# Kernel tuning notes

Hardware: AMD Instinct MI355X
Metric: run time of the kernel (lower is better)

Reference implementation:

```python
import jax, jax.numpy as jnp
import numpy as np

N = 30000   # nodes
E = 600000  # edges (avg degree 20)
H = 128     # hidden_channels
L = 4       # num_layers
G = 64      # graphs in batch


def _init(key, shape, fan_in):
    return (jax.random.normal(key, shape, jnp.float32) / np.sqrt(fan_in)).astype(jnp.float32)


def setup_inputs() -> dict:
    key = jax.random.key(0)
    ks = jax.random.split(key, 24)
    x = jax.random.normal(ks[0], (N, 1), jnp.float32)
    pos = jax.random.normal(ks[1], (N, 3), jnp.float32)
    edge_index = jax.random.randint(ks[2], (2, E), 0, N, dtype=jnp.int32).astype(jnp.int64)
    batch = jnp.sort(jax.random.randint(ks[3], (N,), 0, G, dtype=jnp.int32)).astype(jnp.int64)

    emb_w = _init(ks[4], (1, H), 1)
    emb_b = jnp.zeros((H,), jnp.float32)

    # stacked per-layer params: msg MLP (2H+1 -> H -> H), node MLP (2H -> H -> H)
    msg_w1 = _init(ks[5], (L, 2 * H + 1, H), 2 * H + 1)
    msg_b1 = jnp.zeros((L, H), jnp.float32)
    msg_w2 = _init(ks[6], (L, H, H), H)
    msg_b2 = jnp.zeros((L, H), jnp.float32)
    node_w1 = _init(ks[7], (L, 2 * H, H), 2 * H)
    node_b1 = jnp.zeros((L, H), jnp.float32)
    node_w2 = _init(ks[8], (L, H, H), H)
    node_b2 = jnp.zeros((L, H), jnp.float32)

    out_w1 = _init(ks[9], (H, 32), H)
    out_b1 = jnp.zeros((32,), jnp.float32)
    out_w2 = _init(ks[10], (32, 1), 32)
    out_b2 = jnp.zeros((1,), jnp.float32)

    return {
        "x": x, "pos": pos, "edge_index": edge_index, "batch": batch,
        "emb_w": emb_w, "emb_b": emb_b,
        "msg_w1": msg_w1, "msg_b1": msg_b1, "msg_w2": msg_w2, "msg_b2": msg_b2,
        "node_w1": node_w1, "node_b1": node_b1, "node_w2": node_w2, "node_b2": node_b2,
        "out_w1": out_w1, "out_b1": out_b1, "out_w2": out_w2, "out_b2": out_b2,
    }


def reference(x, pos, edge_index, batch,
              emb_w, emb_b,
              msg_w1, msg_b1, msg_w2, msg_b2,
              node_w1, node_b1, node_w2, node_b2,
              out_w1, out_b1, out_w2, out_b2):
    row, col = edge_index[0], edge_index[1]  # row = source j, col = target i
    # edge scalar: squared distance (computed once, reused across layers)
    dist_sq = jnp.sum((pos[row] - pos[col]) ** 2, axis=-1, keepdims=True)  # [E,1]

    h = x @ emb_w + emb_b  # [N,H]
    for l in range(L):
        x_j = h[row]   # source features
        x_i = h[col]   # target features
        m = jnp.concatenate([x_i, x_j, dist_sq], axis=-1)           # [E, 2H+1]
        m = jax.nn.silu(m @ msg_w1[l] + msg_b1[l]) @ msg_w2[l] + msg_b2[l]  # [E,H]
        aggr = jax.ops.segment_sum(m, col, num_segments=N)          # scatter-add to targets
        nh = jnp.concatenate([h, aggr], axis=-1)                    # [N, 2H]
        h = jax.nn.silu(nh @ node_w1[l] + node_b1[l]) @ node_w2[l] + node_b2[l]
        # dropout omitted for deterministic reference (eval mode)

    g = jax.ops.segment_sum(h, batch, num_segments=G)               # global_add_pool [G,H]
    return jax.nn.silu(g @ out_w1 + out_b1) @ out_w2 + out_b2       # [G,1]
```

## Files before the change

kernel.cpp:

```cpp
#include <hip/hip_runtime.h>

typedef unsigned short u16;
typedef __bf16 bf16x8 __attribute__((ext_vector_type(8)));
typedef float f32x4 __attribute__((ext_vector_type(4)));

#define HN 128
#define TM 64
#define ASTRIDE 136
#define ECH 256

__device__ __forceinline__ u16 f2bf(float f) {
  union { float f; unsigned u; } v; v.f = f;
  unsigned r = v.u + 0x7fffu + ((v.u >> 16) & 1u);
  return (u16)(r >> 16);
}
__device__ __forceinline__ float bf2f(u16 v) {
  union { unsigned u; float f; } x; x.u = ((unsigned)v) << 16; return x.f;
}
__device__ __forceinline__ float bflo(unsigned v) {
  union { unsigned u; float f; } x; x.u = v << 16; return x.f;
}
__device__ __forceinline__ float bfhi(unsigned v) {
  union { unsigned u; float f; } x; x.u = v & 0xffff0000u; return x.f;
}
__device__ __forceinline__ float silu_f(float x) {
  float e = __builtin_amdgcn_exp2f(-1.442695041f * x);
  return x * __builtin_amdgcn_rcpf(1.f + e);
}

__global__ void pack_weights(const float* __restrict__ msg_w1, const float* __restrict__ msg_w2,
                             const float* __restrict__ node_w1, const float* __restrict__ node_w2,
                             u16* __restrict__ pw, int* __restrict__ deg,
                             float* __restrict__ g, int N_, int GH) {
  int id = blockIdx.x * 256 + threadIdx.x;
  if (id < N_) deg[id] = 0;
  if (id < GH) g[id] = 0.f;
  if (id >= 4 * 6 * 16384) return;
  int l = id / (6 * 16384);
  int rem = id % (6 * 16384);
  int m = rem / 16384;
  int e = rem % 16384;
  int kg = e >> 10;
  int n = (e >> 3) & 127;
  int j = e & 7;
  int k = kg * 8 + j;
  float v = 0.f;
  switch (m) {
    case 0: v = msg_w1[(l * 257 + k) * 128 + n]; break;
    case 1: v = msg_w1[(l * 257 + 128 + k) * 128 + n]; break;
    case 2: v = msg_w2[(l * 128 + k) * 128 + n]; break;
    case 3: v = node_w1[(l * 256 + k) * 128 + n]; break;
    case 4: v = node_w1[(l * 256 + 128 + k) * 128 + n]; break;
    case 5: v = node_w2[(l * 128 + k) * 128 + n]; break;
  }
  pw[id] = f2bf(v);
}

__device__ __forceinline__ void gemm64(const u16* s_A, const u16* s_W,
                                       int w, int quad, int m16, f32x4 acc[8]) {
#pragma unroll
  for (int ks = 0; ks < 4; ks++) {
    bf16x8 a = *(const bf16x8*)&s_A[(w * 16 + m16) * ASTRIDE + ks * 32 + quad * 8];
#pragma unroll
    for (int ct = 0; ct < 8; ct++) {
      bf16x8 b = *(const bf16x8*)&s_W[(ks * 4 + quad) * 1024 + (ct * 16 + m16) * 8];
      acc[ct] = __builtin_amdgcn_mfma_f32_16x16x32_bf16(a, b, acc[ct], 0, 0, 0);
    }
  }
}

__global__ __launch_bounds__(256) void fold_kernel(
    const float* __restrict__ msg_w2, const float* __restrict__ node_w1,
    const float* __restrict__ msg_b2, const u16* __restrict__ pw,
    u16* __restrict__ pwc, float* __restrict__ vc) {
  __shared__ __align__(16) u16 s_A[TM * ASTRIDE];
  __shared__ __align__(16) u16 s_W[16384];
  const int t = threadIdx.x;
  const int w = t >> 6, lane = t & 63, quad = lane >> 4, m16 = lane & 15;
  const int b = blockIdx.x, l = b >> 1, half = b & 1;
  const int tile0 = half * 64;

  {
    int r = t >> 2, qo = (t & 3) * 32;
    const float4* src = (const float4*)(msg_w2 + (size_t)(l * 128 + tile0 + r) * 128 + qo);
    u16* dst = s_A + r * ASTRIDE + qo;
#pragma unroll
    for (int i = 0; i < 8; i++) {
      float4 v = src[i];
      ushort4 o;
      o.x = f2bf(v.x); o.y = f2bf(v.y); o.z = f2bf(v.z); o.w = f2bf(v.w);
      *(ushort4*)(dst + i * 4) = o;
    }
  }
  {
    const int4* src = (const int4*)(pw + (size_t)(l * 6 + 4) * 16384);
    int4* dst = (int4*)s_W;
#pragma unroll
    for (int i = 0; i < 8; i++) dst[t + i * 256] = src[t + i * 256];
  }
  __syncthreads();
  f32x4 acc[8];
#pragma unroll
  for (int ct = 0; ct < 8; ct++) acc[ct] = {0.f, 0.f, 0.f, 0.f};
  gemm64(s_A, s_W, w, quad, m16, acc);
#pragma unroll
  for (int ct = 0; ct < 8; ct++)
#pragma unroll
    for (int j = 0; j < 4; j++) {
      int k = tile0 + w * 16 + quad * 4 + j;
      int n = ct * 16 + m16;
      pwc[(size_t)l * 16384 + (k >> 3) * 1024 + n * 8 + (k & 7)] = f2bf(acc[ct][j]);
    }
  if (half == 0 && t < 128) {
    float s = 0.f;
    for (int np = 0; np < 128; np++)
      s += msg_b2[l * 128 + np] * node_w1[(size_t)(l * 256 + 128 + np) * 128 + t];
    vc[l * 128 + t] = s;
  }
}

__global__ void hist_kernel(const int* __restrict__ eidx, int* __restrict__ deg, int E_) {
  int e = blockIdx.x * 256 + threadIdx.x;
  if (e < E_) atomicAdd(&deg[eidx[E_ + e]], 1);
}

__global__ void scan1_kernel(const int* __restrict__ deg, int* __restrict__ off,
                             int* __restrict__ bsum, int n) {
  __shared__ int s[256];
  int t = threadIdx.x;
  int i = blockIdx.x * 256 + t;
  int v = (i < n) ? deg[i] : 0;
  s[t] = v;
  for (int d = 1; d < 256; d <<= 1) {
    __syncthreads();
    int x = (t >= d) ? s[t - d] : 0;
    __syncthreads();
    s[t] += x;
  }
  __syncthreads();
  if (i < n) off[i] = s[t] - v;
  if (t == 255) bsum[blockIdx.x] = s[255];
}

__global__ void scan2_kernel(int* __restrict__ bsum, int nb) {
  __shared__ int s[256];
  int t = threadIdx.x;
  int v = (t < nb) ? bsum[t] : 0;
  s[t] = v;
  for (int d = 1; d < 256; d <<= 1) {
    __syncthreads();
    int x = (t >= d) ? s[t - d] : 0;
    __syncthreads();
    s[t] += x;
  }
  __syncthreads();
  if (t < nb) bsum[t] = s[t] - v;
}

__global__ void scan3_kernel(int* __restrict__ off, const int* __restrict__ bsum,
                             int* __restrict__ cursor, int n) {
  int i = blockIdx.x * 256 + threadIdx.x;
  if (i < n) {
    int v = off[i] + bsum[blockIdx.x];
    off[i] = v;
    cursor[i] = v;
  }
}

__global__ void scatter_kernel(const int* __restrict__ eidx, const float* __restrict__ pos,
                               int* __restrict__ cursor, int4* __restrict__ es16, int E_) {
  int e = blockIdx.x * 256 + threadIdx.x;
  if (e >= E_) return;
  int sr = eidx[e], tg = eidx[E_ + e];
  float dx = pos[sr * 3 + 0] - pos[tg * 3 + 0];
  float dy = pos[sr * 3 + 1] - pos[tg * 3 + 1];
  float dz = pos[sr * 3 + 2] - pos[tg * 3 + 2];
  float d = dx * dx + dy * dy + dz * dz;
  int p = atomicAdd(&cursor[tg], 1);
  int4 v;
  v.x = sr; v.y = tg; v.z = __float_as_int(d); v.w = 0;
  es16[p] = v;
}

__global__ __launch_bounds__(256) void proj_kernel(
    const float* __restrict__ x, const float* __restrict__ emb_w,
    const float* __restrict__ emb_b, u16* __restrict__ hbf,
    u16* __restrict__ Pout, u16* __restrict__ Qout,
    const u16* __restrict__ pw, const float* __restrict__ b1, int nnodes) {
  __shared__ __align__(16) u16 s_A[TM * ASTRIDE];
  __shared__ __align__(16) u16 s_W[16384];
  const int t = threadIdx.x;
  const int w = t >> 6, lane = t & 63, quad = lane >> 4, m16 = lane & 15;
  const int tile0 = blockIdx.x * TM;
  {
    int r = t >> 2, qo = (t & 3) * 32;
    int node = tile0 + r;
    if (node >= nnodes) node = nnodes - 1;
    float xv = x[node];
    u16 hv[32];
#pragma unroll
    for (int i = 0; i < 32; i++) hv[i] = f2bf(xv * emb_w[qo + i] + emb_b[qo + i]);
    u16* dst = s_A + r * ASTRIDE + qo;
#pragma unroll
    for (int i = 0; i < 4; i++) *(int4*)(dst + i * 8) = *(int4*)(hv + i * 8);
    u16* gd = hbf + (size_t)node * HN + qo;
#pragma unroll
    for (int i = 0; i < 4; i++) *(int4*)(gd + i * 8) = *(int4*)(hv + i * 8);
  }
  {
    const int4* src = (const int4*)pw;
    int4* dst = (int4*)s_W;
#pragma unroll
    for (int i = 0; i < 8; i++) dst[t + i * 256] = src[t + i * 256];
  }
  __syncthreads();
  f32x4 acc[8];
#pragma unroll
  for (int ct = 0; ct < 8; ct++) acc[ct] = {0.f, 0.f, 0.f, 0.f};
  gemm64(s_A, s_W, w, quad, m16, acc);
  __syncthreads();
  {
    const int4* src = (const int4*)(pw + 16384);
    int4* dst = (int4*)s_W;
#pragma unroll
    for (int i = 0; i < 8; i++) dst[t + i * 256] = src[t + i * 256];
  }
  float bb[8];
#pragma unroll
  for (int ct = 0; ct < 8; ct++) bb[ct] = b1[ct * 16 + m16];
#pragma unroll
  for (int ct = 0; ct < 8; ct++)
#pragma unroll
    for (int j = 0; j < 4; j++) {
      int n = tile0 + w * 16 + quad * 4 + j;
      if (n < nnodes) Pout[n * HN + ct * 16 + m16] = f2bf(acc[ct][j] + bb[ct]);
    }
  __syncthreads();
#pragma unroll
  for (int ct = 0; ct < 8; ct++) acc[ct] = {0.f, 0.f, 0.f, 0.f};
  gemm64(s_A, s_W, w, quad, m16, acc);
#pragma unroll
  for (int ct = 0; ct < 8; ct++)
#pragma unroll
    for (int j = 0; j < 4; j++) {
      int n = tile0 + w * 16 + quad * 4 + j;
      if (n < nnodes) Qout[n * HN + ct * 16 + m16] = f2bf(acc[ct][j]);
    }
}

__device__ __forceinline__ void edge_step(
    int tg_s, float dd_s, unsigned qv,
    int& cur_s, float& p0, float& p1, float& s0, float& s1,
    const u16* __restrict__ P, float* __restrict__ S, int cp,
    float wd0, float wd1, int tprev_s, int tnext_s) {
  if (tg_s != cur_s) {
    if (cur_s >= 0) {
      float* dst = &S[(size_t)cur_s * HN + cp];
      if (cur_s == tprev_s || cur_s == tnext_s) {
        atomicAdd(dst, s0);
        atomicAdd(dst + 1, s1);
      } else {
        float2 v = {s0, s1};
        *(float2*)dst = v;
      }
    }
    cur_s = tg_s; s0 = 0.f; s1 = 0.f;
    int cg = tg_s < 0 ? 0 : tg_s;
    unsigned pv = *(const unsigned*)&P[(size_t)cg * HN + cp];
    p0 = bflo(pv); p1 = bfhi(pv);
  }
  float x0 = p0 + bflo(qv) + dd_s * wd0;
  float x1 = p1 + bfhi(qv) + dd_s * wd1;
  s0 += silu_f(x0);
  s1 += silu_f(x1);
}

__global__ __launch_bounds__(256) void edge_kernel(
    const u16* __restrict__ P, const u16* __restrict__ Q,
    float* __restrict__ S, const float* __restrict__ w1d,
    const int4* __restrict__ es16, int E_) {
  __shared__ int s_src[ECH + 8];
  __shared__ int s_tgt[ECH + 8];
  __shared__ float s_dist[ECH + 8];

  const int t = threadIdx.x;
  const int e0 = blockIdx.x * ECH;
  {
    int e = e0 + t;
    if (e < E_) {
      int4 v = es16[e];
      s_src[t] = v.x;
      s_tgt[t] = v.y;
      s_dist[t] = __int_as_float(v.z);
    } else {
      s_src[t] = 0; s_tgt[t] = -1; s_dist[t] = 0.f;
    }
    if (t < 8) { s_src[ECH + t] = 0; s_tgt[ECH + t] = -1; s_dist[ECH + t] = 0.f; }
  }
  __syncthreads();

  const int lane = t & 63;
  const int w = t >> 6;
  const int cp = lane * 2;
  const int a = w * 64;
  const float2 wdv = *(const float2*)&w1d[cp];
  const float wd0 = wdv.x, wd1 = wdv.y;

  int tprev_s, tnext_s;
  if (w == 0) tprev_s = (e0 > 0) ? es16[e0 - 1].y : -2;
  else tprev_s = s_tgt[a - 1];
  if (w == 3) tnext_s = (e0 + ECH < E_) ? es16[e0 + ECH].y : -2;
  else tnext_s = s_tgt[a + 64];
  tprev_s = __builtin_amdgcn_readfirstlane(tprev_s);
  tnext_s = __builtin_amdgcn_readfirstlane(tnext_s);

  int tg[8];
  float dd[8];
  unsigned qv[8];
#pragma unroll
  for (int j = 0; j < 8; j++) {
    tg[j] = s_tgt[a + j];
    dd[j] = s_dist[a + j];
    qv[j] = *(const unsigned*)&Q[(size_t)s_src[a + j] * HN + cp];
  }

  int cur_s = -1;
  float s0 = 0.f, s1 = 0.f, p0 = 0.f, p1 = 0.f;

#pragma unroll
  for (int i = a; i < a + 64; i += 8) {
    int tgn[8];
    float ddn[8];
    unsigned qvn[8];
#pragma unroll
    for (int j = 0; j < 8; j++) {
      int idx = i + 8 + j;
      tgn[j] = s_tgt[idx];
      ddn[j] = s_dist[idx];
      qvn[j] = *(const unsigned*)&Q[(size_t)s_src[idx] * HN + cp];
    }
#pragma unroll
    for (int j = 0; j < 8; j++) {
      int tg_s = __builtin_amdgcn_readfirstlane(tg[j]);
      float dd_s = __builtin_amdgcn_readfirstlane(__float_as_int(dd[j])) != 0
                       ? dd[j] : dd[j];
      edge_step(tg_s, dd[j], qv[j], cur_s, p0, p1, s0, s1, P, S, cp, wd0, wd1, tprev_s, tnext_s);
      (void)dd_s;
    }
#pragma unroll
    for (int j = 0; j < 8; j++) { tg[j] = tgn[j]; dd[j] = ddn[j]; qv[j] = qvn[j]; }
  }

  if (cur_s >= 0) {
    float* dst = &S[(size_t)cur_s * HN + cp];
    if (cur_s == tprev_s || cur_s == tnext_s) {
      atomicAdd(dst, s0);
      atomicAdd(dst + 1, s1);
    } else {
      float2 v = {s0, s1};
      *(float2*)dst = v;
    }
  }
}

template <bool FUSE>
__global__ __launch_bounds__(256) void node_kernel(
    const u16* __restrict__ hbf, float* __restrict__ S, const int* __restrict__ deg,
    u16* __restrict__ hout, const u16* __restrict__ pwc, const float* __restrict__ vc,
    const u16* __restrict__ pwn, const float* __restrict__ b1, const float* __restrict__ b2,
    const u16* __restrict__ pw_next, const float* __restrict__ b1_next,
    u16* __restrict__ Pout, u16* __restrict__ Qout, int nnodes) {
  __shared__ __align__(16) u16 s_A[TM * ASTRIDE];
  __shared__ __align__(16) u16 s_W[16384];
  const int t = threadIdx.x;
  const int w = t >> 6, lane = t & 63, quad = lane >> 4, m16 = lane & 15;
  const int tile0 = blockIdx.x * TM;
  const int r_ = t >> 2, qo_ = (t & 3) * 32;
  int node_ = tile0 + r_;
  if (node_ >= nnodes) node_ = nnodes - 1;

  {
    const int4* src = (const int4*)pwc;
    int4* dst = (int4*)s_W;
#pragma unroll
    for (int i = 0; i < 8; i++) dst[t + i * 256] = src[t + i * 256];
  }
  {
    const float4* src = (const float4*)(S + (size_t)node_ * HN + qo_);
    u16* dst = s_A + r_ * ASTRIDE + qo_;
#pragma unroll
    for (int i = 0; i < 8; i++) {
      float4 v = src[i];
      ushort4 o;
      o.x = f2bf(v.x); o.y = f2bf(v.y); o.z = f2bf(v.z); o.w = f2bf(v.w);
      *(ushort4*)(dst + i * 4) = o;
    }
    float4 z = {0.f, 0.f, 0.f, 0.f};
    float4* zd = (float4*)(S + (size_t)node_ * HN + qo_);
#pragma unroll
    for (int i = 0; i < 8; i++) zd[i] = z;
  }
  __syncthreads();

  f32x4 acc[8];
#pragma unroll
  for (int ct = 0; ct < 8; ct++) acc[ct] = {0.f, 0.f, 0.f, 0.f};
  gemm64(s_A, s_W, w, quad, m16, acc);
  __syncthreads();

  {
    const int4* src = (const int4*)pwn;
    int4* dst = (int4*)s_W;
#pragma unroll
    for (int i = 0; i < 8; i++) dst[t + i * 256] = src[t + i * 256];
  }
  {
    const int4* src = (const int4*)(hbf + (size_t)node_ * HN + qo_);
    int4* dst = (int4*)(s_A + r_ * ASTRIDE + qo_);
#pragma unroll
    for (int i = 0; i < 4; i++) dst[i] = src[i];
  }
  __syncthreads();
  gemm64(s_A, s_W, w, quad, m16, acc);
  __syncthreads();

  {
    const int4* src = (const int4*)(pwn + 32768);
    int4* dst = (int4*)s_W;
#pragma unroll
    for (int i = 0; i < 8; i++) dst[t + i * 256] = src[t + i * 256];
  }
  {
    float bb1[8], vcr[8];
#pragma unroll
    for (int ct = 0; ct < 8; ct++) {
      bb1[ct] = b1[ct * 16 + m16];
      vcr[ct] = vc[ct * 16 + m16];
    }
    float degv[4];
#pragma unroll
    for (int j = 0; j < 4; j++) {
      int n = tile0 + w * 16 + quad * 4 + j;
      if (n >= nnodes) n = nnodes - 1;
      degv[j] = (float)deg[n];
    }
#pragma unroll
    for (int ct = 0; ct < 8; ct++)
#pragma unroll
      for (int j = 0; j < 4; j++) {
        int row = w * 16 + quad * 4 + j;
        float xv = acc[ct][j] + bb1[ct] + degv[j] * vcr[ct];
        s_A[row * ASTRIDE + ct * 16 + m16] = f2bf(silu_f(xv));
      }
  }
  __syncthreads();

#pragma unroll
  for (int ct = 0; ct < 8; ct++) acc[ct] = {0.f, 0.f, 0.f, 0.f};
  gemm64(s_A, s_W, w, quad, m16, acc);

  float bb2[8];
#pragma unroll
  for (int ct = 0; ct < 8; ct++) bb2[ct] = b2[ct * 16 + m16];
#pragma unroll
  for (int ct = 0; ct < 8; ct++)
#pragma unroll
    for (int j = 0; j < 4; j++) {
      int row = w * 16 + quad * 4 + j;
      int n = tile0 + row;
      if (n < nnodes) hout[n * HN + ct * 16 + m16] = f2bf(acc[ct][j] + bb2[ct]);
    }

  if (FUSE) {
#pragma unroll
    for (int ct = 0; ct < 8; ct++)
#pragma unroll
      for (int j = 0; j < 4; j++) {
        int row = w * 16 + quad * 4 + j;
        s_A[row * ASTRIDE + ct * 16 + m16] = f2bf(acc[ct][j] + bb2[ct]);
      }
    __syncthreads();
    {
      const int4* src = (const int4*)pw_next;
      int4* dst = (int4*)s_W;
#pragma unroll
      for (int i = 0; i < 8; i++) dst[t + i * 256] = src[t + i * 256];
    }
    __syncthreads();
#pragma unroll
    for (int ct = 0; ct < 8; ct++) acc[ct] = {0.f, 0.f, 0.f, 0.f};
    gemm64(s_A, s_W, w, quad, m16, acc);
    {
      float bbn[8];
#pragma unroll
      for (int ct = 0; ct < 8; ct++) bbn[ct] = b1_next[ct * 16 + m16];
#pragma unroll
      for (int ct = 0; ct < 8; ct++)
#pragma unroll
        for (int j = 0; j < 4; j++) {
          int n = tile0 + w * 16 + quad * 4 + j;
          if (n < nnodes) Pout[n * HN + ct * 16 + m16] = f2bf(acc[ct][j] + bbn[ct]);
        }
    }
    __syncthreads();
    {
      const int4* src = (const int4*)(pw_next + 16384);
      int4* dst = (int4*)s_W;
#pragma unroll
      for (int i = 0; i < 8; i++) dst[t + i * 256] = src[t + i * 256];
    }
    __syncthreads();
#pragma unroll
    for (int ct = 0; ct < 8; ct++) acc[ct] = {0.f, 0.f, 0.f, 0.f};
    gemm64(s_A, s_W, w, quad, m16, acc);
#pragma unroll
    for (int ct = 0; ct < 8; ct++)
#pragma unroll
      for (int j = 0; j < 4; j++) {
        int n = tile0 + w * 16 + quad * 4 + j;
        if (n < nnodes) Qout[n * HN + ct * 16 + m16] = f2bf(acc[ct][j]);
      }
  }
}

__global__ __launch_bounds__(256) void pool_kernel(
    const u16* __restrict__ h, const int* __restrict__ batch,
    float* __restrict__ g, int N) {
  __shared__ int s_b[64];
  const int t = threadIdx.x;
  const int n0 = blockIdx.x * 64;
  if (t < 64) {
    int n = n0 + t;
    s_b[t] = (n < N) ? batch[n] : -1;
  }
  __syncthreads();
  const int cp = (t & 63) * 2;
  const int rg = t >> 6;
  int cur = -1;
  float s0 = 0.f, s1 = 0.f;
#pragma unroll 4
  for (int i = 0; i < 16; i++) {
    int r = rg * 16 + i;
    int b = s_b[r];
    if (b < 0) break;
    if (b != cur) {
      if (cur >= 0) {
        atomicAdd(&g[cur * HN + cp], s0);
        atomicAdd(&g[cur * HN + cp + 1], s1);
      }
      cur = b; s0 = 0.f; s1 = 0.f;
    }
    unsigned v = *(const unsigned*)&h[(size_t)(n0 + r) * HN + cp];
    s0 += bf2f((u16)(v & 0xffffu));
    s1 += bf2f((u16)(v >> 16));
  }
  if (cur >= 0) {
    atomicAdd(&g[cur * HN + cp], s0);
    atomicAdd(&g[cur * HN + cp + 1], s1);
  }
}

__global__ __launch_bounds__(64) void out_kernel(
    const float* __restrict__ g, const float* __restrict__ w1,
    const float* __restrict__ b1, const float* __restrict__ w2,
    const float* __restrict__ b2, float* __restrict__ out) {
  const int gi = blockIdx.x;
  const int t = threadIdx.x;
  const int c = t & 31, kh = t >> 5;
  float s = 0.f;
  for (int k = kh * 64; k < kh * 64 + 64; k++)
    s += g[gi * HN + k] * w1[k * 32 + c];
  s += __shfl_down(s, 32);
  float r = 0.f;
  if (kh == 0) r = silu_f(s + b1[c]) * w2[c];
  r += __shfl_down(r, 16);
  r += __shfl_down(r, 8);
  r += __shfl_down(r, 4);
  r += __shfl_down(r, 2);
  r += __shfl_down(r, 1);
  if (t == 0) out[gi] = r + b2[0];
}

extern "C" void kernel_launch(void* const* d_in, const int* in_sizes, int n_in,
                              void* d_out, int out_size, void* d_ws, size_t ws_size,
                              hipStream_t stream) {
  const float* x = (const float*)d_in[0];
  const float* pos = (const float*)d_in[1];
  const int* eidx = (const int*)d_in[2];
  const int* batch = (const int*)d_in[3];
  const float* emb_w = (const float*)d_in[4];
  const float* emb_b = (const float*)d_in[5];
  const float* msg_w1 = (const float*)d_in[6];
  const float* msg_b1 = (const float*)d_in[7];
  const float* msg_w2 = (const float*)d_in[8];
  const float* msg_b2 = (const float*)d_in[9];
  const float* node_w1 = (const float*)d_in[10];
  const float* node_b1 = (const float*)d_in[11];
  const float* node_w2 = (const float*)d_in[12];
  const float* node_b2 = (const float*)d_in[13];
  const float* out_w1 = (const float*)d_in[14];
  const float* out_b1 = (const float*)d_in[15];
  const float* out_w2 = (const float*)d_in[16];
  const float* out_b2 = (const float*)d_in[17];
  float* outp = (float*)d_out;

  const int N = 30000, E = 600000, G = 64;
  const size_t NH = (size_t)N * HN;

  u16* hA = (u16*)d_ws;
  u16* hB = hA + NH;
  u16* Pp = hB + NH;
  u16* Qp = Pp + NH;
  float* S = (float*)(Qp + NH);
  int4* es16 = (int4*)(S + NH);
  int* deg = (int*)(es16 + E);
  int* off = deg + N;
  int* cursor = off + N;
  int* bsum = cursor + N;
  float* g = (float*)(bsum + 128);
  u16* pw = (u16*)(g + G * HN);
  u16* pwc = pw + (size_t)4 * 6 * 16384;
  float* vcb = (float*)(pwc + (size_t)4 * 16384);

  const int NB = (N + 255) / 256;
  const int NTB = (N + TM - 1) / TM;

  pack_weights<<<(4 * 6 * 16384 + 255) / 256, 256, 0, stream>>>(
      msg_w1, msg_w2, node_w1, node_w2, pw, deg, g, N, G * HN);
  fold_kernel<<<8, 256, 0, stream>>>(msg_w2, node_w1, msg_b2, pw, pwc, vcb);

  hist_kernel<<<(E + 255) / 256, 256, 0, stream>>>(eidx, deg, E);
  scan1_kernel<<<NB, 256, 0, stream>>>(deg, off, bsum, N);
  scan2_kernel<<<1, 256, 0, stream>>>(bsum, NB);
  scan3_kernel<<<NB, 256, 0, stream>>>(off, bsum, cursor, N);
  scatter_kernel<<<(E + 255) / 256, 256, 0, stream>>>(eidx, pos, cursor, es16, E);

  hipMemsetAsync(S, 0, NH * sizeof(float), stream);

  proj_kernel<<<NTB, 256, 0, stream>>>(x, emb_w, emb_b, hA, Pp, Qp, pw, msg_b1, N);

  u16* hcur = hA;
  u16* hnext = hB;
  for (int l = 0; l < 4; l++) {
    const u16* pwl = pw + (size_t)(l * 6) * 16384;
    edge_kernel<<<(E + ECH - 1) / ECH, 256, 0, stream>>>(
        Pp, Qp, S,
        msg_w1 + (size_t)(l * 257 + 256) * 128,
        es16, E);
    if (l < 3) {
      const u16* pw_next = pw + (size_t)((l + 1) * 6) * 16384;
      node_kernel<true><<<NTB, 256, 0, stream>>>(
          hcur, S, deg, hnext, pwc + (size_t)l * 16384, vcb + l * 128,
          pwl + 3 * 16384, node_b1 + l * 128, node_b2 + l * 128,
          pw_next, msg_b1 + (l + 1) * 128, Pp, Qp, N);
    } else {
      node_kernel<false><<<NTB, 256, 0, stream>>>(
          hcur, S, deg, hnext, pwc + (size_t)l * 16384, vcb + l * 128,
          pwl + 3 * 16384, node_b1 + l * 128, node_b2 + l * 128,
          nullptr, nullptr, nullptr, nullptr, N);
    }
    u16* tmp = hcur; hcur = hnext; hnext = tmp;
  }

  pool_kernel<<<(N + 63) / 64, 256, 0, stream>>>(hcur, batch, g, N);
  out_kernel<<<G, 64, 0, stream>>>(g, out_w1, out_b1, out_w2, out_b2, outp);
}
```

Baseline: 420.0 us.

## Fuse edge aggregation into node kernel with shared-memory CSR accumulation

Merges the separate edge kernel into the per-layer node kernel. Each 64-node tile walks its CSR edge range and accumulates messages into a shared-memory buffer with LDS atomics, replacing the global S buffer, its memset and the global atomics. P/Q are double-buffered because the fused kernel now writes next-layer projections while other blocks still read the current ones. Per-block edge work is now tied to the tile's degree sum, and each wave handles only a quarter of the tile's edges, which may lower latency hiding compared with the old edge-parallel grid.

```diff
diff --git a/kernel.cpp b/kernel.cpp
--- a/kernel.cpp
+++ b/kernel.cpp
@@ -7,7 +7,7 @@
 #define HN 128
 #define TM 64
 #define ASTRIDE 136
-#define ECH 256
+#define SSTRIDE 132
 
 __device__ __forceinline__ u16 f2bf(float f) {
   union { float f; unsigned u; } v; v.f = f;
@@ -248,157 +248,113 @@
     }
 }
 
-__device__ __forceinline__ void edge_step(
-    int tg_s, float dd_s, unsigned qv,
-    int& cur_s, float& p0, float& p1, float& s0, float& s1,
-    const u16* __restrict__ P, float* __restrict__ S, int cp,
-    float wd0, float wd1, int tprev_s, int tnext_s) {
-  if (tg_s != cur_s) {
-    if (cur_s >= 0) {
-      float* dst = &S[(size_t)cur_s * HN + cp];
-      if (cur_s == tprev_s || cur_s == tnext_s) {
-        atomicAdd(dst, s0);
-        atomicAdd(dst + 1, s1);
-      } else {
-        float2 v = {s0, s1};
-        *(float2*)dst = v;
-      }
-    }
-    cur_s = tg_s; s0 = 0.f; s1 = 0.f;
-    int cg = tg_s < 0 ? 0 : tg_s;
-    unsigned pv = *(const unsigned*)&P[(size_t)cg * HN + cp];
-    p0 = bflo(pv); p1 = bfhi(pv);
-  }
-  float x0 = p0 + bflo(qv) + dd_s * wd0;
-  float x1 = p1 + bfhi(qv) + dd_s * wd1;
-  s0 += silu_f(x0);
-  s1 += silu_f(x1);
-}
-
-__global__ __launch_bounds__(256) void edge_kernel(
-    const u16* __restrict__ P, const u16* __restrict__ Q,
-    float* __restrict__ S, const float* __restrict__ w1d,
-    const int4* __restrict__ es16, int E_) {
-  __shared__ int s_src[ECH + 8];
-  __shared__ int s_tgt[ECH + 8];
-  __shared__ float s_dist[ECH + 8];
-
-  const int t = threadIdx.x;
-  const int e0 = blockIdx.x * ECH;
-  {
-    int e = e0 + t;
-    if (e < E_) {
-      int4 v = es16[e];
-      s_src[t] = v.x;
-      s_tgt[t] = v.y;
-      s_dist[t] = __int_as_float(v.z);
-    } else {
-      s_src[t] = 0; s_tgt[t] = -1; s_dist[t] = 0.f;
-    }
-    if (t < 8) { s_src[ECH + t] = 0; s_tgt[ECH + t] = -1; s_dist[ECH + t] = 0.f; }
-  }
-  __syncthreads();
-
-  const int lane = t & 63;
-  const int w = t >> 6;
-  const int cp = lane * 2;
-  const int a = w * 64;
-  const float2 wdv = *(const float2*)&w1d[cp];
-  const float wd0 = wdv.x, wd1 = wdv.y;
-
-  int tprev_s, tnext_s;
-  if (w == 0) tprev_s = (e0 > 0) ? es16[e0 - 1].y : -2;
-  else tprev_s = s_tgt[a - 1];
-  if (w == 3) tnext_s = (e0 + ECH < E_) ? es16[e0 + ECH].y : -2;
-  else tnext_s = s_tgt[a + 64];
-  tprev_s = __builtin_amdgcn_readfirstlane(tprev_s);
-  tnext_s = __builtin_amdgcn_readfirstlane(tnext_s);
-
-  int tg[8];
-  float dd[8];
-  unsigned qv[8];
-#pragma unroll
-  for (int j = 0; j < 8; j++) {
-    tg[j] = s_tgt[a + j];
-    dd[j] = s_dist[a + j];
-    qv[j] = *(const unsigned*)&Q[(size_t)s_src[a + j] * HN + cp];
-  }
-
-  int cur_s = -1;
-  float s0 = 0.f, s1 = 0.f, p0 = 0.f, p1 = 0.f;
-
-#pragma unroll
-  for (int i = a; i < a + 64; i += 8) {
-    int tgn[8];
-    float ddn[8];
-    unsigned qvn[8];
-#pragma unroll
-    for (int j = 0; j < 8; j++) {
-      int idx = i + 8 + j;
-      tgn[j] = s_tgt[idx];
-      ddn[j] = s_dist[idx];
-      qvn[j] = *(const unsigned*)&Q[(size_t)s_src[idx] * HN + cp];
-    }
-#pragma unroll
-    for (int j = 0; j < 8; j++) {
-      int tg_s = __builtin_amdgcn_readfirstlane(tg[j]);
-      float dd_s = __builtin_amdgcn_readfirstlane(__float_as_int(dd[j])) != 0
-                       ? dd[j] : dd[j];
-      edge_step(tg_s, dd[j], qv[j], cur_s, p0, p1, s0, s1, P, S, cp, wd0, wd1, tprev_s, tnext_s);
-      (void)dd_s;
-    }
-#pragma unroll
-    for (int j = 0; j < 8; j++) { tg[j] = tgn[j]; dd[j] = ddn[j]; qv[j] = qvn[j]; }
-  }
-
-  if (cur_s >= 0) {
-    float* dst = &S[(size_t)cur_s * HN + cp];
-    if (cur_s == tprev_s || cur_s == tnext_s) {
-      atomicAdd(dst, s0);
-      atomicAdd(dst + 1, s1);
-    } else {
-      float2 v = {s0, s1};
-      *(float2*)dst = v;
-    }
-  }
-}
-
 template <bool FUSE>
-__global__ __launch_bounds__(256) void node_kernel(
-    const u16* __restrict__ hbf, float* __restrict__ S, const int* __restrict__ deg,
+__global__ __launch_bounds__(256) void layer_kernel(
+    const u16* __restrict__ hbf, const int* __restrict__ deg, const int* __restrict__ off,
+    const int4* __restrict__ es16,
+    const u16* __restrict__ P, const u16* __restrict__ Q, const float* __restrict__ w1d,
     u16* __restrict__ hout, const u16* __restrict__ pwc, const float* __restrict__ vc,
     const u16* __restrict__ pwn, const float* __restrict__ b1, const float* __restrict__ b2,
     const u16* __restrict__ pw_next, const float* __restrict__ b1_next,
-    u16* __restrict__ Pout, u16* __restrict__ Qout, int nnodes) {
+    u16* __restrict__ Pout, u16* __restrict__ Qout, int nnodes, int E_) {
   __shared__ __align__(16) u16 s_A[TM * ASTRIDE];
-  __shared__ __align__(16) u16 s_W[16384];
+  __shared__ __align__(16) char s_buf[TM * SSTRIDE * 4];
+  float* s_S = (float*)s_buf;
+  u16* s_W = (u16*)s_buf;
+
   const int t = threadIdx.x;
   const int w = t >> 6, lane = t & 63, quad = lane >> 4, m16 = lane & 15;
+  const int cp = lane * 2;
   const int tile0 = blockIdx.x * TM;
   const int r_ = t >> 2, qo_ = (t & 3) * 32;
   int node_ = tile0 + r_;
   if (node_ >= nnodes) node_ = nnodes - 1;
 
+  for (int i = t; i < TM * SSTRIDE; i += 256) s_S[i] = 0.f;
+  const int e_start = off[tile0];
+  const int e_end = (tile0 + TM < nnodes) ? off[tile0 + TM] : E_;
+  __syncthreads();
+
+  {
+    const float2 wdv = *(const float2*)&w1d[cp];
+    const float wd0 = wdv.x, wd1 = wdv.y;
+    const int len = e_end - e_start;
+    const int a = e_start + (len * w) / 4;
+    const int b = e_start + (len * (w + 1)) / 4;
+    if (a < b) {
+      int cur_s = -1, cur_r = 0;
+      float s0 = 0.f, s1 = 0.f, p0 = 0.f, p1 = 0.f;
+      int4 v[4];
+      unsigned qv[4];
+#pragma unroll
+      for (int j = 0; j < 4; j++) {
+        int e = a + j; if (e >= b) e = b - 1;
+        v[j] = es16[e];
+      }
+#pragma unroll
+      for (int j = 0; j < 4; j++)
+        qv[j] = *(const unsigned*)&Q[(size_t)v[j].x * HN + cp];
+
+      for (int e = a; e < b; e += 4) {
+        int4 vn[4];
+        unsigned qn[4];
+#pragma unroll
+        for (int j = 0; j < 4; j++) {
+          int en = e + 4 + j; if (en >= b) en = b - 1;
+          vn[j] = es16[en];
+        }
+#pragma unroll
+        for (int j = 0; j < 4; j++)
+          qn[j] = *(const unsigned*)&Q[(size_t)vn[j].x * HN + cp];
+#pragma unroll
+        for (int j = 0; j < 4; j++) {
+          if (e + j < b) {
+            int tg_s = __builtin_amdgcn_readfirstlane(v[j].y);
+            float dd = __int_as_float(v[j].z);
+            if (tg_s != cur_s) {
+              if (cur_s >= 0) {
+                atomicAdd(&s_S[cur_r * SSTRIDE + cp], s0);
+                atomicAdd(&s_S[cur_r * SSTRIDE + cp + 1], s1);
+              }
+              cur_s = tg_s; cur_r = tg_s - tile0; s0 = 0.f; s1 = 0.f;
+              unsigned pv = *(const unsigned*)&P[(size_t)tg_s * HN + cp];
+              p0 = bflo(pv); p1 = bfhi(pv);
+            }
+            float x0 = p0 + bflo(qv[j]) + dd * wd0;
+            float x1 = p1 + bfhi(qv[j]) + dd * wd1;
+            s0 += silu_f(x0);
+            s1 += silu_f(x1);
+          }
+        }
+#pragma unroll
+        for (int j = 0; j < 4; j++) { v[j] = vn[j]; qv[j] = qn[j]; }
+      }
+      if (cur_s >= 0) {
+        atomicAdd(&s_S[cur_r * SSTRIDE + cp], s0);
+        atomicAdd(&s_S[cur_r * SSTRIDE + cp + 1], s1);
+      }
+    }
+  }
+  __syncthreads();
+
+  {
+    const float* srow = s_S + r_ * SSTRIDE + qo_;
+    u16* dst = s_A + r_ * ASTRIDE + qo_;
+#pragma unroll
+    for (int i = 0; i < 8; i++) {
+      float4 v4 = *(const float4*)(srow + i * 4);
+      ushort4 o;
+      o.x = f2bf(v4.x); o.y = f2bf(v4.y); o.z = f2bf(v4.z); o.w = f2bf(v4.w);
+      *(ushort4*)(dst + i * 4) = o;
+    }
+  }
+  __syncthreads();
+
   {
     const int4* src = (const int4*)pwc;
     int4* dst = (int4*)s_W;
 #pragma unroll
     for (int i = 0; i < 8; i++) dst[t + i * 256] = src[t + i * 256];
-  }
-  {
-    const float4* src = (const float4*)(S + (size_t)node_ * HN + qo_);
-    u16* dst = s_A + r_ * ASTRIDE + qo_;
-#pragma unroll
-    for (int i = 0; i < 8; i++) {
-      float4 v = src[i];
-      ushort4 o;
-      o.x = f2bf(v.x); o.y = f2bf(v.y); o.z = f2bf(v.z); o.w = f2bf(v.w);
-      *(ushort4*)(dst + i * 4) = o;
-    }
-    float4 z = {0.f, 0.f, 0.f, 0.f};
-    float4* zd = (float4*)(S + (size_t)node_ * HN + qo_);
-#pragma unroll
-    for (int i = 0; i < 8; i++) zd[i] = z;
   }
   __syncthreads();
 
@@ -609,10 +565,11 @@
 
   u16* hA = (u16*)d_ws;
   u16* hB = hA + NH;
-  u16* Pp = hB + NH;
-  u16* Qp = Pp + NH;
-  float* S = (float*)(Qp + NH);
-  int4* es16 = (int4*)(S + NH);
+  u16* PpA = hB + NH;
+  u16* QpA = PpA + NH;
+  u16* PpB = QpA + NH;
+  u16* QpB = PpB + NH;
+  int4* es16 = (int4*)(QpB + NH);
   int* deg = (int*)(es16 + E);
   int* off = deg + N;
   int* cursor = off + N;
@@ -635,29 +592,30 @@
   scan3_kernel<<<NB, 256, 0, stream>>>(off, bsum, cursor, N);
   scatter_kernel<<<(E + 255) / 256, 256, 0, stream>>>(eidx, pos, cursor, es16, E);
 
-  hipMemsetAsync(S, 0, NH * sizeof(float), stream);
-
-  proj_kernel<<<NTB, 256, 0, stream>>>(x, emb_w, emb_b, hA, Pp, Qp, pw, msg_b1, N);
+  proj_kernel<<<NTB, 256, 0, stream>>>(x, emb_w, emb_b, hA, PpA, QpA, pw, msg_b1, N);
 
   u16* hcur = hA;
   u16* hnext = hB;
   for (int l = 0; l < 4; l++) {
     const u16* pwl = pw + (size_t)(l * 6) * 16384;
-    edge_kernel<<<(E + ECH - 1) / ECH, 256, 0, stream>>>(
-        Pp, Qp, S,
-        msg_w1 + (size_t)(l * 257 + 256) * 128,
-        es16, E);
+    const u16* Pcur = (l & 1) ? PpB : PpA;
+    const u16* Qcur = (l & 1) ? QpB : QpA;
+    u16* Pnxt = (l & 1) ? PpA : PpB;
+    u16* Qnxt = (l & 1) ? QpA : QpB;
+    const float* w1d_l = msg_w1 + (size_t)(l * 257 + 256) * 128;
     if (l < 3) {
       const u16* pw_next = pw + (size_t)((l + 1) * 6) * 16384;
-      node_kernel<true><<<NTB, 256, 0, stream>>>(
-          hcur, S, deg, hnext, pwc + (size_t)l * 16384, vcb + l * 128,
+      layer_kernel<true><<<NTB, 256, 0, stream>>>(
+          hcur, deg, off, es16, Pcur, Qcur, w1d_l, hnext,
+          pwc + (size_t)l * 16384, vcb + l * 128,
           pwl + 3 * 16384, node_b1 + l * 128, node_b2 + l * 128,
-          pw_next, msg_b1 + (l + 1) * 128, Pp, Qp, N);
+          pw_next, msg_b1 + (l + 1) * 128, Pnxt, Qnxt, N, E);
     } else {
-      node_kernel<false><<<NTB, 256, 0, stream>>>(
-          hcur, S, deg, hnext, pwc + (size_t)l * 16384, vcb + l * 128,
+      layer_kernel<false><<<NTB, 256, 0, stream>>>(
+          hcur, deg, off, es16, Pcur, Qcur, w1d_l, hnext,
+          pwc + (size_t)l * 16384, vcb + l * 128,
           pwl + 3 * 16384, node_b1 + l * 128, node_b2 + l * 128,
-          nullptr, nullptr, nullptr, nullptr, N);
+          nullptr, nullptr, nullptr, nullptr, N, E);
     }
     u16* tmp = hcur; hcur = hnext; hnext = tmp;
   }
```

Result: slower. 551.6 us (+31.3%).
